# Kernel tuning notes

Measured on AMD Instinct MI355X. Metric: run time of the kernel, lower is better.

Reference implementation:

```python
import jax, jax.numpy as jnp
import numpy as np

N_ATOMS = 100000
N_BONDS = 2000000
F = 32  # fixed feature width implied by hardcoded MLP input dims


def _linear_init(key, din, dout):
    kw, kb = jax.random.split(key)
    s = 1.0 / np.sqrt(din)
    w = jax.random.uniform(kw, (din, dout), jnp.float32, -s, s)
    b = jax.random.uniform(kb, (dout,), jnp.float32, -s, s)
    return w, b


def _mlp(x, w1, b1, w2, b2, w3, b3):
    # Linear(din,64)-SELU-Linear(64,64)-SELU-Linear(64,32)-SELU
    x = jax.nn.selu(x @ w1 + b1)
    x = jax.nn.selu(x @ w2 + b2)
    return jax.nn.selu(x @ w3 + b3)


def setup_inputs() -> dict:
    key = jax.random.key(0)
    ks = jax.random.split(key, 14)
    inp = {
        "bonds": jax.random.normal(ks[0], (N_BONDS, F), jnp.float32),
        "bond_atom_1": jax.random.randint(ks[1], (N_BONDS,), 0, N_ATOMS, jnp.int32),
        "bond_atom_2": jax.random.randint(ks[2], (N_BONDS,), 0, N_ATOMS, jnp.int32),
        "atoms": jax.random.normal(ks[3], (N_ATOMS, F), jnp.float32),
        "state": jax.random.normal(ks[4], (1, F), jnp.float32),
    }
    # phi_e: 128 -> 64 -> 64 -> 32
    inp["e_w1"], inp["e_b1"] = _linear_init(ks[5], 128, 64)
    inp["e_w2"], inp["e_b2"] = _linear_init(ks[6], 64, 64)
    inp["e_w3"], inp["e_b3"] = _linear_init(ks[7], 64, 32)
    # phi_v: 96 -> 64 -> 64 -> 32
    inp["v_w1"], inp["v_b1"] = _linear_init(ks[8], 96, 64)
    inp["v_w2"], inp["v_b2"] = _linear_init(ks[9], 64, 64)
    inp["v_w3"], inp["v_b3"] = _linear_init(ks[10], 64, 32)
    # phi_u: 96 -> 64 -> 64 -> 32
    inp["u_w1"], inp["u_b1"] = _linear_init(ks[11], 96, 64)
    inp["u_w2"], inp["u_b2"] = _linear_init(ks[12], 64, 64)
    inp["u_w3"], inp["u_b3"] = _linear_init(ks[13], 64, 32)
    return inp


def reference(bonds, bond_atom_1, bond_atom_2, atoms, state,
              e_w1, e_b1, e_w2, e_b2, e_w3, e_b3,
              v_w1, v_b1, v_w2, v_b2, v_w3, v_b3,
              u_w1, u_b1, u_w2, u_b2, u_w3, u_b3):
    n_bonds = bonds.shape[0]
    n_atoms = atoms.shape[0]
    state_b = jnp.broadcast_to(state, (n_bonds, state.shape[1]))
    # gather atom features per bond endpoint
    a1 = atoms[bond_atom_1]  # [E, F]
    a2 = atoms[bond_atom_2]  # [E, F]
    bonds_new = _mlp(jnp.concatenate([a1, a2, bonds, state_b], axis=1),
                     e_w1, e_b1, e_w2, e_b2, e_w3, e_b3)  # [E, 32]
    # scatter-add bond messages back to atom 1, normalize by bond count
    b2a = jax.ops.segment_sum(bonds_new, bond_atom_1, num_segments=n_atoms)  # [N, 32]
    cnt = jax.ops.segment_sum(jnp.ones((n_bonds,), bonds_new.dtype), bond_atom_1,
                              num_segments=n_atoms)  # [N]
    b2a = b2a / cnt[:, None]
    state_a = jnp.broadcast_to(state, (n_atoms, state.shape[1]))
    atoms_new = _mlp(jnp.concatenate([b2a, atoms, state_a], axis=1),
                     v_w1, v_b1, v_w2, v_b2, v_w3, v_b3)  # [N, 32]
    state_new = _mlp(jnp.concatenate([jnp.mean(bonds_new, axis=0, keepdims=True),
                                      jnp.mean(atoms_new, axis=0, keepdims=True),
                                      state], axis=1),
                     u_w1, u_b1, u_w2, u_b2, u_w3, u_b3)  # [1, 32]
    return bonds_new, atoms_new, state_new
```

## Files before the change

kernel.cpp:

```cpp
#include <hip/hip_runtime.h>
#include <math.h>

typedef __attribute__((ext_vector_type(4))) int    int4v;
typedef __attribute__((ext_vector_type(4))) float  float4v;
typedef __attribute__((ext_vector_type(8))) __bf16 bf16x8;

#define SCAN_BLK 1024
#define EBLK 512

static constexpr float SELU_SCALE = 1.0507009873554805f;
static constexpr float SELU_ALPHA = 1.6732632423543772f;

__device__ __forceinline__ float selu_f(float x) {
    const float sa = SELU_SCALE * SELU_ALPHA;
    float e = __expf(x);
    return x > 0.0f ? SELU_SCALE * x : fmaf(sa, e, -sa);
}

__device__ __forceinline__ unsigned short f2bf(float f) {
    uint32_t u = __builtin_bit_cast(uint32_t, f);
    return (unsigned short)((u + 0x7FFFu + ((u >> 16) & 1u)) >> 16);
}

__device__ __forceinline__ uint32_t pk2(float a, float b) {
    uint32_t r;
    asm("v_cvt_pk_bf16_f32 %0, %1, %2" : "=v"(r) : "v"(a), "v"(b));
    return r;
}

__device__ __forceinline__ float4v mfma_bf16(int4v a, int4v b, float4v c) {
    return __builtin_amdgcn_mfma_f32_16x16x32_bf16(
        __builtin_bit_cast(bf16x8, a), __builtin_bit_cast(bf16x8, b), c, 0, 0, 0);
}


__global__ __launch_bounds__(256) void cnt_kernel(const int* __restrict__ ba1,
                                                  int* __restrict__ cnt, int nb) {
    for (int e = blockIdx.x * 256 + threadIdx.x; e < nb; e += gridDim.x * 256)
        atomicAdd(cnt + ba1[e], 1);
}

__global__ __launch_bounds__(SCAN_BLK) void scan_block_kernel(const int* __restrict__ cnt,
                                                              int* __restrict__ excl,
                                                              int* __restrict__ bsums, int na) {
    __shared__ int tmp[SCAN_BLK];
    const int t = threadIdx.x;
    const int base = blockIdx.x * SCAN_BLK;
    const int v = (base + t < na) ? cnt[base + t] : 0;
    tmp[t] = v;
    __syncthreads();
    for (int off = 1; off < SCAN_BLK; off <<= 1) {
        const int add = (t >= off) ? tmp[t - off] : 0;
        __syncthreads();
        tmp[t] += add;
        __syncthreads();
    }
    if (base + t < na) excl[base + t] = tmp[t] - v;
    if (t == SCAN_BLK - 1) bsums[blockIdx.x] = tmp[t];
}

__global__ void scan_tops_kernel(const int* __restrict__ bsums, int* __restrict__ bases,
                                 int nblocks) {
    if (threadIdx.x == 0 && blockIdx.x == 0) {
        int s = 0;
        for (int bk = 0; bk < nblocks; ++bk) { bases[bk] = s; s += bsums[bk]; }
    }
}

__global__ __launch_bounds__(256) void wcur_init_kernel(const int* __restrict__ excl,
                                                        const int* __restrict__ bases,
                                                        int* __restrict__ wcur, int na) {
    const int a = blockIdx.x * 256 + threadIdx.x;
    if (a < na) wcur[a] = bases[a >> 10] + excl[a];
}


__global__ void bias_prep_kernel(const float* __restrict__ state,
                                 const float* __restrict__ ew1, const float* __restrict__ eb1,
                                 const float* __restrict__ vw1, const float* __restrict__ vb1,
                                 float* __restrict__ ebias, float* __restrict__ vbias) {
    const int t = threadIdx.x;
    if (t >= 64) return;
    if (blockIdx.x == 0) {
        float acc = eb1[t];
        for (int k = 0; k < 32; ++k) acc = fmaf(state[k], ew1[(96 + k) * 64 + t], acc);
        ebias[t] = acc;
    } else {
        float acc = vb1[t];
        for (int k = 0; k < 32; ++k) acc = fmaf(state[k], vw1[(64 + k) * 64 + t], acc);
        vbias[t] = acc;
    }
}


__global__ __launch_bounds__(256) void aprep_kernel(const float* __restrict__ atoms,
                                                    unsigned short* __restrict__ abf,
                                                    int nel8) {
    const int i = blockIdx.x * 256 + threadIdx.x;
    if (i >= nel8) return;
    const float* p = atoms + (size_t)i * 8;
    uint4 v;
    v.x = pk2(p[0], p[1]); v.y = pk2(p[2], p[3]);
    v.z = pk2(p[4], p[5]); v.w = pk2(p[6], p[7]);
    *(uint4*)(abf + (size_t)i * 8) = v;
}

__global__ __launch_bounds__(256) void wprep_kernel(
    const float* __restrict__ ew1, const float* __restrict__ ew2, const float* __restrict__ ew3,
    const float* __restrict__ vw1, const float* __restrict__ vw2, const float* __restrict__ vw3,
    unsigned short* __restrict__ wfe, unsigned short* __restrict__ wfv)
{
    const int idx = blockIdx.x * 256 + threadIdx.x;
    if (idx >= 44 * 64) return;
    const int fid = idx >> 6, lane = idx & 63;
    const int b = lane & 15, g = lane >> 4;
    const float* W; int N, t, c;
    if (fid < 12)      { W = ew1; N = 64; t = fid / 3;        c = fid % 3; }
    else if (fid < 20) { W = ew2; N = 64; t = (fid - 12) / 2; c = (fid - 12) % 2; }
    else if (fid < 24) { W = ew3; N = 32; t = (fid - 20) / 2; c = (fid - 20) % 2; }
    else if (fid < 32) { W = vw1; N = 64; t = (fid - 24) / 2; c = (fid - 24) % 2; }
    else if (fid < 40) { W = vw2; N = 64; t = (fid - 32) / 2; c = (fid - 32) % 2; }
    else               { W = vw3; N = 32; t = (fid - 40) / 2; c = (fid - 40) % 2; }
    unsigned short* dst = (fid < 24) ? (wfe + fid * 512) : (wfv + (fid - 24) * 512);
    for (int j = 0; j < 8; ++j) {
        const float w = W[(size_t)(32 * c + 8 * g + j) * N + 16 * t + b];
        dst[lane * 8 + j] = f2bf(w);
    }
}


__global__ __launch_bounds__(EBLK, 8) void phi_e_mfma(
    const float* __restrict__ bonds, const int* __restrict__ ba1, const int* __restrict__ ba2,
    const unsigned short* __restrict__ abf,
    const unsigned short* __restrict__ wfe, const float* __restrict__ ebias,
    const float* __restrict__ eb2, const float* __restrict__ eb3,
    float* __restrict__ out, int* __restrict__ wcur, int* __restrict__ list, int nb)
{
    __shared__ __align__(16) char lds[25344 + (EBLK / 64) * 2048];
    {
        const uint4* src = (const uint4*)wfe;
        uint4* dst = (uint4*)lds;
        #pragma unroll
        for (int i = 0; i < 3; ++i) dst[threadIdx.x + i * EBLK] = src[threadIdx.x + i * EBLK];
        float* bd = (float*)(lds + 24576);
        const int t = threadIdx.x;
        if (t < 64)        bd[t] = ebias[t];
        else if (t < 128)  bd[t] = eb2[t - 64];
        else if (t < 160)  bd[t] = eb3[t - 128];
    }
    __syncthreads();

    const char* wl = lds;
    const float* bias_l = (const float*)(lds + 24576);
    const int tid = threadIdx.x;
    const int wid = tid >> 6, lane = tid & 63;
    const int b = lane & 15, g = lane >> 4;
    char* hb = lds + 25344 + wid * 2048;
    const uint32_t swz = (uint32_t)((b & 7) << 4);
    const uint32_t row = (uint32_t)(b * 128);
    const uint32_t loff = (uint32_t)(lane * 16);

    const int ntile = (nb + 15) >> 4;
    const int stride = gridDim.x * (EBLK / 64);

    for (int m = blockIdx.x * (EBLK / 64) + wid; m < ntile; m += stride) {
        const int e0 = m << 4;
        const int er = min(e0 + b, nb - 1);
        const int i1 = ba1[er], i2 = ba2[er];

        if (g == 0 && e0 + b < nb) {
            const int pos = atomicAdd(wcur + i1, 1);
            __builtin_nontemporal_store(er, list + pos);
        }

        const int4v xa1 = *(const int4v*)(abf + (size_t)i1 * 32 + 8 * g);
        const int4v xa2 = *(const int4v*)(abf + (size_t)i2 * 32 + 8 * g);
        int4v xb;
        {
            const float* p = bonds + (size_t)er * 32 + 8 * g;
            const float4v u0 = __builtin_nontemporal_load((const float4v*)p);
            const float4v u1 = __builtin_nontemporal_load((const float4v*)p + 1);
            xb[0] = (int)pk2(u0.x, u0.y); xb[1] = (int)pk2(u0.z, u0.w);
            xb[2] = (int)pk2(u1.x, u1.y); xb[3] = (int)pk2(u1.z, u1.w);
        }

        float4v acc[4];
        #pragma unroll
        for (int t = 0; t < 4; ++t) acc[t] = *(const float4v*)(bias_l + 16 * t + 4 * g);
        #pragma unroll
        for (int t = 0; t < 4; ++t) {
            acc[t] = mfma_bf16(*(const int4v*)(wl + (t * 3 + 0) * 1024 + loff), xa1, acc[t]);
            acc[t] = mfma_bf16(*(const int4v*)(wl + (t * 3 + 1) * 1024 + loff), xa2, acc[t]);
            acc[t] = mfma_bf16(*(const int4v*)(wl + (t * 3 + 2) * 1024 + loff), xb,  acc[t]);
        }
        #pragma unroll
        for (int t = 0; t < 4; ++t) {
            const float s0 = selu_f(acc[t][0]), s1 = selu_f(acc[t][1]);
            const float s2 = selu_f(acc[t][2]), s3 = selu_f(acc[t][3]);
            const uint32_t q = (uint32_t)(t * 32 + g * 8);
            *(uint2*)(hb + row + (q ^ swz)) = make_uint2(pk2(s0, s1), pk2(s2, s3));
        }
        int4v xh0 = *(const int4v*)(hb + row + (((uint32_t)(g * 16)) ^ swz));
        int4v xh1 = *(const int4v*)(hb + row + (((uint32_t)(64 + g * 16)) ^ swz));

        #pragma unroll
        for (int t = 0; t < 4; ++t) acc[t] = *(const float4v*)(bias_l + 64 + 16 * t + 4 * g);
        #pragma unroll
        for (int t = 0; t < 4; ++t) {
            acc[t] = mfma_bf16(*(const int4v*)(wl + (12 + t * 2 + 0) * 1024 + loff), xh0, acc[t]);
            acc[t] = mfma_bf16(*(const int4v*)(wl + (12 + t * 2 + 1) * 1024 + loff), xh1, acc[t]);
        }
        #pragma unroll
        for (int t = 0; t < 4; ++t) {
            const float s0 = selu_f(acc[t][0]), s1 = selu_f(acc[t][1]);
            const float s2 = selu_f(acc[t][2]), s3 = selu_f(acc[t][3]);
            const uint32_t q = (uint32_t)(t * 32 + g * 8);
            *(uint2*)(hb + row + (q ^ swz)) = make_uint2(pk2(s0, s1), pk2(s2, s3));
        }
        xh0 = *(const int4v*)(hb + row + (((uint32_t)(g * 16)) ^ swz));
        xh1 = *(const int4v*)(hb + row + (((uint32_t)(64 + g * 16)) ^ swz));

        float4v acc3[2];
        acc3[0] = *(const float4v*)(bias_l + 128 + 4 * g);
        acc3[1] = *(const float4v*)(bias_l + 128 + 16 + 4 * g);
        #pragma unroll
        for (int t = 0; t < 2; ++t) {
            acc3[t] = mfma_bf16(*(const int4v*)(wl + (20 + t * 2 + 0) * 1024 + loff), xh0, acc3[t]);
            acc3[t] = mfma_bf16(*(const int4v*)(wl + (20 + t * 2 + 1) * 1024 + loff), xh1, acc3[t]);
        }
        if (e0 + b < nb) {
            #pragma unroll
            for (int t = 0; t < 2; ++t) {
                float4v ov;
                ov.x = selu_f(acc3[t][0]); ov.y = selu_f(acc3[t][1]);
                ov.z = selu_f(acc3[t][2]); ov.w = selu_f(acc3[t][3]);
                *(float4v*)(out + (size_t)(e0 + b) * 32 + 16 * t + 4 * g) = ov;
            }
        }
    }
}


__global__ __launch_bounds__(256) void gather_mean_kernel(
    const float* __restrict__ bonds_new, const int* __restrict__ list,
    const int* __restrict__ excl, const int* __restrict__ bases,
    const int* __restrict__ cnt, float* __restrict__ mean,
    float* __restrict__ bpart, int na)
{
    __shared__ float red[4][32];
    const int idx = blockIdx.x * 256 + threadIdx.x;
    const int a = idx >> 3, q = idx & 7;
    float4v s = {0.f, 0.f, 0.f, 0.f};
    int n = 0;
    if (a < na) {
        const int start = bases[a >> 10] + excl[a];
        n = cnt[a];
        const int end = start + n;
        float4v s1 = {0.f, 0.f, 0.f, 0.f};
        float4v s2 = {0.f, 0.f, 0.f, 0.f};
        float4v s3 = {0.f, 0.f, 0.f, 0.f};
        int p = start;
        for (; p + 4 <= end; p += 4) {
            const int e0 = list[p], e1 = list[p + 1], e2 = list[p + 2], e3 = list[p + 3];
            s  += *(const float4v*)(bonds_new + (size_t)e0 * 32 + q * 4);
            s1 += *(const float4v*)(bonds_new + (size_t)e1 * 32 + q * 4);
            s2 += *(const float4v*)(bonds_new + (size_t)e2 * 32 + q * 4);
            s3 += *(const float4v*)(bonds_new + (size_t)e3 * 32 + q * 4);
        }
        for (; p < end; ++p)
            s += *(const float4v*)(bonds_new + (size_t)list[p] * 32 + q * 4);
        s = (s + s1) + (s2 + s3);
    }

    {
        float4v t = s;
        #pragma unroll
        for (int off = 8; off < 64; off <<= 1) {
            t.x += __shfl_xor(t.x, off); t.y += __shfl_xor(t.y, off);
            t.z += __shfl_xor(t.z, off); t.w += __shfl_xor(t.w, off);
        }
        const int wv = threadIdx.x >> 6;
        const int lane = threadIdx.x & 63;
        if (lane < 8) {
            red[wv][lane * 4 + 0] = t.x; red[wv][lane * 4 + 1] = t.y;
            red[wv][lane * 4 + 2] = t.z; red[wv][lane * 4 + 3] = t.w;
        }
        __syncthreads();
        if (threadIdx.x < 32) {
            const int f = threadIdx.x;
            bpart[(size_t)blockIdx.x * 32 + f] =
                red[0][f] + red[1][f] + red[2][f] + red[3][f];
        }
    }

    if (a < na) {
        const float inv = 1.0f / (float)n;
        *(float4v*)(mean + (size_t)a * 32 + q * 4) = s * inv;
    }
}


__global__ __launch_bounds__(1024) void part_reduce_kernel(const float* __restrict__ part,
                                                           float* __restrict__ dst, int nblk) {
    __shared__ float red[32][33];
    const int f = threadIdx.x & 31;
    const int c = threadIdx.x >> 5;
    float s = 0.0f;
    for (int i = c; i < nblk; i += 32) s += part[(size_t)i * 32 + f];
    red[c][f] = s;
    __syncthreads();
    if (threadIdx.x < 32) {
        float t = 0.0f;
        #pragma unroll
        for (int c2 = 0; c2 < 32; ++c2) t += red[c2][threadIdx.x];
        dst[threadIdx.x] = t;
    }
}


__global__ __launch_bounds__(256) void phi_v_mfma(
    const unsigned short* __restrict__ abf, float* __restrict__ out ,
    const unsigned short* __restrict__ wfv, const float* __restrict__ vbias,
    const float* __restrict__ vb2, const float* __restrict__ vb3,
    float* __restrict__ apart, int na)
{
    __shared__ __align__(16) char lds_raw[4 * 2048];
    __shared__ float redv[4][32];
    const int tid = threadIdx.x;
    const int wid = tid >> 6, lane = tid & 63;
    const int b = lane & 15, g = lane >> 4;
    char* hb = lds_raw + wid * 2048;
    const uint32_t swz = (uint32_t)((b & 7) << 4);
    const uint32_t row = (uint32_t)(b * 128);

    int4v wv1[4][2], wv2[4][2], wv3[2][2];
    #pragma unroll
    for (int t = 0; t < 4; ++t)
        #pragma unroll
        for (int c = 0; c < 2; ++c) {
            wv1[t][c] = *(const int4v*)(wfv + (t * 2 + c) * 512 + lane * 8);
            wv2[t][c] = *(const int4v*)(wfv + (8 + t * 2 + c) * 512 + lane * 8);
        }
    #pragma unroll
    for (int t = 0; t < 2; ++t)
        #pragma unroll
        for (int c = 0; c < 2; ++c)
            wv3[t][c] = *(const int4v*)(wfv + (16 + t * 2 + c) * 512 + lane * 8);

    float ssum[8];
    #pragma unroll
    for (int i = 0; i < 8; ++i) ssum[i] = 0.0f;

    const int ntile = (na + 15) >> 4;
    const int m = blockIdx.x * 4 + wid;
    if (m < ntile) {
        const int a0 = m << 4;
        const int ar = (a0 + b < na) ? (a0 + b) : (na - 1);

        int4v xm;
        {
            const float* p = out + (size_t)ar * 32 + 8 * g;
            const float4v u0 = *(const float4v*)p, u1 = *(const float4v*)(p + 4);
            xm[0] = (int)pk2(u0.x, u0.y); xm[1] = (int)pk2(u0.z, u0.w);
            xm[2] = (int)pk2(u1.x, u1.y); xm[3] = (int)pk2(u1.z, u1.w);
        }
        const int4v xa = *(const int4v*)(abf + (size_t)ar * 32 + 8 * g);

        float4v acc[4];
        #pragma unroll
        for (int t = 0; t < 4; ++t) acc[t] = *(const float4v*)(vbias + 16 * t + 4 * g);
        #pragma unroll
        for (int t = 0; t < 4; ++t) {
            acc[t] = mfma_bf16(wv1[t][0], xm, acc[t]);
            acc[t] = mfma_bf16(wv1[t][1], xa, acc[t]);
        }
        #pragma unroll
        for (int t = 0; t < 4; ++t) {
            const float s0 = selu_f(acc[t][0]), s1 = selu_f(acc[t][1]);
            const float s2 = selu_f(acc[t][2]), s3 = selu_f(acc[t][3]);
            const uint32_t q = (uint32_t)(t * 32 + g * 8);
            *(uint2*)(hb + row + (q ^ swz)) = make_uint2(pk2(s0, s1), pk2(s2, s3));
        }
        int4v xh0 = *(const int4v*)(hb + row + (((uint32_t)(g * 16)) ^ swz));
        int4v xh1 = *(const int4v*)(hb + row + (((uint32_t)(64 + g * 16)) ^ swz));

        #pragma unroll
        for (int t = 0; t < 4; ++t) acc[t] = *(const float4v*)(vb2 + 16 * t + 4 * g);
        #pragma unroll
        for (int t = 0; t < 4; ++t) {
            acc[t] = mfma_bf16(wv2[t][0], xh0, acc[t]);
            acc[t] = mfma_bf16(wv2[t][1], xh1, acc[t]);
        }
        #pragma unroll
        for (int t = 0; t < 4; ++t) {
            const float s0 = selu_f(acc[t][0]), s1 = selu_f(acc[t][1]);
            const float s2 = selu_f(acc[t][2]), s3 = selu_f(acc[t][3]);
            const uint32_t q = (uint32_t)(t * 32 + g * 8);
            *(uint2*)(hb + row + (q ^ swz)) = make_uint2(pk2(s0, s1), pk2(s2, s3));
        }
        xh0 = *(const int4v*)(hb + row + (((uint32_t)(g * 16)) ^ swz));
        xh1 = *(const int4v*)(hb + row + (((uint32_t)(64 + g * 16)) ^ swz));

        float4v acc3[2];
        acc3[0] = *(const float4v*)(vb3 + 4 * g);
        acc3[1] = *(const float4v*)(vb3 + 16 + 4 * g);
        #pragma unroll
        for (int t = 0; t < 2; ++t) {
            acc3[t] = mfma_bf16(wv3[t][0], xh0, acc3[t]);
            acc3[t] = mfma_bf16(wv3[t][1], xh1, acc3[t]);
        }
        if (a0 + b < na) {
            #pragma unroll
            for (int t = 0; t < 2; ++t) {
                const float o0 = selu_f(acc3[t][0]), o1 = selu_f(acc3[t][1]);
                const float o2 = selu_f(acc3[t][2]), o3 = selu_f(acc3[t][3]);
                float4v ov; ov.x = o0; ov.y = o1; ov.z = o2; ov.w = o3;
                *(float4v*)(out + (size_t)(a0 + b) * 32 + 16 * t + 4 * g) = ov;
                ssum[t * 4 + 0] += o0; ssum[t * 4 + 1] += o1;
                ssum[t * 4 + 2] += o2; ssum[t * 4 + 3] += o3;
            }
        }
    }

    #pragma unroll
    for (int i = 0; i < 8; ++i) {
        float v = ssum[i];
        v += __shfl_xor(v, 1); v += __shfl_xor(v, 2);
        v += __shfl_xor(v, 4); v += __shfl_xor(v, 8);
        if (b == 0) redv[wid][16 * (i >> 2) + 4 * g + (i & 3)] = v;
    }
    __syncthreads();
    if (tid < 32)
        apart[(size_t)blockIdx.x * 32 + tid] =
            redv[0][tid] + redv[1][tid] + redv[2][tid] + redv[3][tid];
}


__global__ __launch_bounds__(128) void phi_u_kernel(
    const float* __restrict__ bsum, const float* __restrict__ asum,
    const float* __restrict__ state,
    const float* __restrict__ w1, const float* __restrict__ b1,
    const float* __restrict__ w2, const float* __restrict__ b2,
    const float* __restrict__ w3, const float* __restrict__ b3,
    float* __restrict__ out, float inv_nb, float inv_na)
{
    __shared__ float x[96];
    __shared__ float hs[64];
    const int t = threadIdx.x;
    if (t < 32)       x[t] = bsum[t] * inv_nb;
    else if (t < 64)  x[t] = asum[t - 32] * inv_na;
    else if (t < 96)  x[t] = state[t - 64];
    __syncthreads();
    if (t < 64) {
        float acc = b1[t];
        for (int k = 0; k < 96; ++k) acc = fmaf(x[k], w1[k * 64 + t], acc);
        hs[t] = selu_f(acc);
    }
    __syncthreads();
    float acc2 = 0.0f;
    if (t < 64) {
        acc2 = b2[t];
        for (int k = 0; k < 64; ++k) acc2 = fmaf(hs[k], w2[k * 64 + t], acc2);
        acc2 = selu_f(acc2);
    }
    __syncthreads();
    if (t < 64) hs[t] = acc2;
    __syncthreads();
    if (t < 32) {
        float acc = b3[t];
        for (int k = 0; k < 64; ++k) acc = fmaf(hs[k], w3[k * 32 + t], acc);
        out[t] = selu_f(acc);
    }
}

extern "C" void kernel_launch(void* const* d_in, const int* in_sizes, int n_in,
                              void* d_out, int out_size, void* d_ws, size_t ws_size,
                              hipStream_t stream) {
    const float* bonds = (const float*)d_in[0];
    const int*   ba1   = (const int*)d_in[1];
    const int*   ba2   = (const int*)d_in[2];
    const float* atoms = (const float*)d_in[3];
    const float* state = (const float*)d_in[4];
    const float* ew1 = (const float*)d_in[5];  const float* eb1 = (const float*)d_in[6];
    const float* ew2 = (const float*)d_in[7];  const float* eb2 = (const float*)d_in[8];
    const float* ew3 = (const float*)d_in[9];  const float* eb3 = (const float*)d_in[10];
    const float* vw1 = (const float*)d_in[11]; const float* vb1 = (const float*)d_in[12];
    const float* vw2 = (const float*)d_in[13]; const float* vb2 = (const float*)d_in[14];
    const float* vw3 = (const float*)d_in[15]; const float* vb3 = (const float*)d_in[16];
    const float* uw1 = (const float*)d_in[17]; const float* ub1 = (const float*)d_in[18];
    const float* uw2 = (const float*)d_in[19]; const float* ub2 = (const float*)d_in[20];
    const float* uw3 = (const float*)d_in[21]; const float* ub3 = (const float*)d_in[22];

    const int nb = in_sizes[1];
    const int na = in_sizes[3] / 32;
    const int nscan = (na + SCAN_BLK - 1) / SCAN_BLK;
    const int ngather = ((na * 8) + 255) / 256;
    const int ntv = (na + 15) / 16;
    const int nvblk = (ntv + 3) / 4;

    float* out       = (float*)d_out;
    float* bonds_out = out;
    float* atoms_out = out + (size_t)nb * 32;
    float* state_out = atoms_out + (size_t)na * 32;

    char* ws = (char*)d_ws;
    size_t off = 0;
    auto alloc = [&](size_t bytes) { char* p = ws + off; off += (bytes + 255) & ~(size_t)255; return p; };
    int*   cnt   = (int*)alloc((size_t)na * 4);
    const size_t zero_bytes = off;
    float* bsum  = (float*)alloc(32 * 4);
    float* asum  = (float*)alloc(32 * 4);
    float* ebias = (float*)alloc(64 * 4);
    float* vbias = (float*)alloc(64 * 4);
    int*   excl  = (int*)alloc((size_t)na * 4);
    int*   bsums = (int*)alloc(128 * 4);
    int*   bases = (int*)alloc(128 * 4);
    int*   wcur  = (int*)alloc((size_t)na * 4);
    int*   list  = (int*)alloc((size_t)nb * 4);
    float* bpart = (float*)alloc((size_t)ngather * 32 * 4);
    float* apart = (float*)alloc((size_t)nvblk * 32 * 4);
    unsigned short* wfe = (unsigned short*)alloc(24 * 512 * 2);
    unsigned short* wfv = (unsigned short*)alloc(20 * 512 * 2);
    unsigned short* abf = (unsigned short*)alloc((size_t)na * 32 * 2);

    (void)hipMemsetAsync(d_ws, 0, zero_bytes, stream);

    bias_prep_kernel<<<2, 64, 0, stream>>>(state, ew1, eb1, vw1, vb1, ebias, vbias);
    wprep_kernel<<<(44 * 64 + 255) / 256, 256, 0, stream>>>(ew1, ew2, ew3, vw1, vw2, vw3,
                                                            wfe, wfv);
    aprep_kernel<<<(na * 4 + 255) / 256, 256, 0, stream>>>(atoms, abf, na * 4);

    cnt_kernel<<<2048, 256, 0, stream>>>(ba1, cnt, nb);
    scan_block_kernel<<<nscan, SCAN_BLK, 0, stream>>>(cnt, excl, bsums, na);
    scan_tops_kernel<<<1, 64, 0, stream>>>(bsums, bases, nscan);
    wcur_init_kernel<<<(na + 255) / 256, 256, 0, stream>>>(excl, bases, wcur, na);

    phi_e_mfma<<<1024, EBLK, 0, stream>>>(bonds, ba1, ba2, abf, wfe, ebias, eb2, eb3,
                                          bonds_out, wcur, list, nb);

    gather_mean_kernel<<<ngather, 256, 0, stream>>>(bonds_out, list, excl, bases, cnt,
                                                    atoms_out, bpart, na);
    part_reduce_kernel<<<1, 1024, 0, stream>>>(bpart, bsum, ngather);

    phi_v_mfma<<<nvblk, 256, 0, stream>>>(abf, atoms_out, wfv, vbias, vb2, vb3,
                                          apart, na);
    part_reduce_kernel<<<1, 1024, 0, stream>>>(apart, asum, nvblk);

    phi_u_kernel<<<1, 128, 0, stream>>>(bsum, asum, state,
                                        uw1, ub1, uw2, ub2, uw3, ub3,
                                        state_out, 1.0f / (float)nb, 1.0f / (float)na);
}
```

Before: 442.6 us.

## Scatter bf16 bond outputs into atom-sorted buffer for contiguous segment gather

In the edge MLP kernel, each bond's output is also written as bf16 into a permuted buffer at its CSR slot, instead of writing an index list. The segment-mean kernel then reads contiguous bf16 rows rather than doing indirect fp32 gathers through the list. The last-layer weights are kept in registers, which shrinks the LDS footprint. The trade-off is an extra scattered write per bond and bf16 rounding in the segment sums, and the path depends on having enough workspace.

```diff
diff --git a/kernel.cpp b/kernel.cpp
--- a/kernel.cpp
+++ b/kernel.cpp
@@ -1,6 +1,7 @@
 #include <hip/hip_runtime.h>
 #include <math.h>
 
+typedef __attribute__((ext_vector_type(2))) unsigned int uint2v;
 typedef __attribute__((ext_vector_type(4))) int    int4v;
 typedef __attribute__((ext_vector_type(4))) float  float4v;
 typedef __attribute__((ext_vector_type(8))) __bf16 bf16x8;
@@ -26,6 +27,13 @@
     uint32_t r;
     asm("v_cvt_pk_bf16_f32 %0, %1, %2" : "=v"(r) : "v"(a), "v"(b));
     return r;
+}
+
+__device__ __forceinline__ float bflo(uint32_t u) {
+    return __builtin_bit_cast(float, u << 16);
+}
+__device__ __forceinline__ float bfhi(uint32_t u) {
+    return __builtin_bit_cast(float, u & 0xFFFF0000u);
 }
 
 __device__ __forceinline__ float4v mfma_bf16(int4v a, int4v b, float4v c) {
@@ -129,20 +137,21 @@
 }
 
 
+template<bool PERM>
 __global__ __launch_bounds__(EBLK, 8) void phi_e_mfma(
     const float* __restrict__ bonds, const int* __restrict__ ba1, const int* __restrict__ ba2,
     const unsigned short* __restrict__ abf,
     const unsigned short* __restrict__ wfe, const float* __restrict__ ebias,
     const float* __restrict__ eb2, const float* __restrict__ eb3,
-    float* __restrict__ out, int* __restrict__ wcur, int* __restrict__ list, int nb)
+    float* __restrict__ out, unsigned short* __restrict__ perm,
+    int* __restrict__ wcur, int* __restrict__ list, int nb)
 {
-    __shared__ __align__(16) char lds[25344 + (EBLK / 64) * 2048];
+    __shared__ __align__(16) char lds[21248 + (EBLK / 64) * 2048];
     {
         const uint4* src = (const uint4*)wfe;
         uint4* dst = (uint4*)lds;
-        #pragma unroll
-        for (int i = 0; i < 3; ++i) dst[threadIdx.x + i * EBLK] = src[threadIdx.x + i * EBLK];
-        float* bd = (float*)(lds + 24576);
+        for (int i = threadIdx.x; i < 1280; i += EBLK) dst[i] = src[i];
+        float* bd = (float*)(lds + 20480);
         const int t = threadIdx.x;
         if (t < 64)        bd[t] = ebias[t];
         else if (t < 128)  bd[t] = eb2[t - 64];
@@ -151,14 +160,21 @@
     __syncthreads();
 
     const char* wl = lds;
-    const float* bias_l = (const float*)(lds + 24576);
+    const float* bias_l = (const float*)(lds + 20480);
     const int tid = threadIdx.x;
     const int wid = tid >> 6, lane = tid & 63;
     const int b = lane & 15, g = lane >> 4;
-    char* hb = lds + 25344 + wid * 2048;
+    char* hb = lds + 21248 + wid * 2048;
     const uint32_t swz = (uint32_t)((b & 7) << 4);
     const uint32_t row = (uint32_t)(b * 128);
     const uint32_t loff = (uint32_t)(lane * 16);
+
+    int4v we3[2][2];
+    #pragma unroll
+    for (int t = 0; t < 2; ++t)
+        #pragma unroll
+        for (int c = 0; c < 2; ++c)
+            we3[t][c] = *(const int4v*)(wfe + (20 + t * 2 + c) * 512 + lane * 8);
 
     const int ntile = (nb + 15) >> 4;
     const int stride = gridDim.x * (EBLK / 64);
@@ -168,9 +184,10 @@
         const int er = min(e0 + b, nb - 1);
         const int i1 = ba1[er], i2 = ba2[er];
 
-        if (g == 0 && e0 + b < nb) {
-            const int pos = atomicAdd(wcur + i1, 1);
-            __builtin_nontemporal_store(er, list + pos);
+        int pos = 0;
+        if (lane < 16 && e0 + b < nb) {
+            pos = atomicAdd(wcur + i1, 1);
+            if (!PERM) __builtin_nontemporal_store(er, list + pos);
         }
 
         const int4v xa1 = *(const int4v*)(abf + (size_t)i1 * 32 + 8 * g);
@@ -225,18 +242,86 @@
         acc3[1] = *(const float4v*)(bias_l + 128 + 16 + 4 * g);
         #pragma unroll
         for (int t = 0; t < 2; ++t) {
-            acc3[t] = mfma_bf16(*(const int4v*)(wl + (20 + t * 2 + 0) * 1024 + loff), xh0, acc3[t]);
-            acc3[t] = mfma_bf16(*(const int4v*)(wl + (20 + t * 2 + 1) * 1024 + loff), xh1, acc3[t]);
-        }
+            acc3[t] = mfma_bf16(we3[t][0], xh0, acc3[t]);
+            acc3[t] = mfma_bf16(we3[t][1], xh1, acc3[t]);
+        }
+
+        if (PERM) pos = __shfl(pos, b);
+
         if (e0 + b < nb) {
             #pragma unroll
             for (int t = 0; t < 2; ++t) {
-                float4v ov;
-                ov.x = selu_f(acc3[t][0]); ov.y = selu_f(acc3[t][1]);
-                ov.z = selu_f(acc3[t][2]); ov.w = selu_f(acc3[t][3]);
-                *(float4v*)(out + (size_t)(e0 + b) * 32 + 16 * t + 4 * g) = ov;
+                const float o0 = selu_f(acc3[t][0]), o1 = selu_f(acc3[t][1]);
+                const float o2 = selu_f(acc3[t][2]), o3 = selu_f(acc3[t][3]);
+                float4v ov; ov.x = o0; ov.y = o1; ov.z = o2; ov.w = o3;
+                if (PERM) {
+                    __builtin_nontemporal_store(ov,
+                        (float4v*)(out + (size_t)(e0 + b) * 32 + 16 * t + 4 * g));
+                    uint2v pv; pv.x = pk2(o0, o1); pv.y = pk2(o2, o3);
+                    *((uint2v*)(perm + (size_t)pos * 32) + (4 * t + g)) = pv;
+                } else {
+                    *(float4v*)(out + (size_t)(e0 + b) * 32 + 16 * t + 4 * g) = ov;
+                }
             }
         }
+    }
+}
+
+
+__global__ __launch_bounds__(256) void gather_perm_kernel(
+    const unsigned short* __restrict__ perm,
+    const int* __restrict__ excl, const int* __restrict__ bases,
+    const int* __restrict__ cnt, float* __restrict__ mean,
+    float* __restrict__ bpart, int na)
+{
+    __shared__ float red[4][32];
+    const int idx = blockIdx.x * 256 + threadIdx.x;
+    const int a = idx >> 3, q = idx & 7;
+    float4v s = {0.f, 0.f, 0.f, 0.f};
+    int n = 0;
+    if (a < na) {
+        const int start = bases[a >> 10] + excl[a];
+        n = cnt[a];
+        float4v s1 = {0.f, 0.f, 0.f, 0.f};
+        const unsigned short* base = perm + (size_t)start * 32 + q * 4;
+        int j = 0;
+        for (; j + 2 <= n; j += 2) {
+            const uint2v v0 = *(const uint2v*)(base + (size_t)j * 32);
+            const uint2v v1 = *(const uint2v*)(base + (size_t)(j + 1) * 32);
+            s.x += bflo(v0.x);  s.y += bfhi(v0.x);  s.z += bflo(v0.y);  s.w += bfhi(v0.y);
+            s1.x += bflo(v1.x); s1.y += bfhi(v1.x); s1.z += bflo(v1.y); s1.w += bfhi(v1.y);
+        }
+        if (j < n) {
+            const uint2v v0 = *(const uint2v*)(base + (size_t)j * 32);
+            s.x += bflo(v0.x); s.y += bfhi(v0.x); s.z += bflo(v0.y); s.w += bfhi(v0.y);
+        }
+        s += s1;
+    }
+
+    {
+        float4v t = s;
+        #pragma unroll
+        for (int off = 8; off < 64; off <<= 1) {
+            t.x += __shfl_xor(t.x, off); t.y += __shfl_xor(t.y, off);
+            t.z += __shfl_xor(t.z, off); t.w += __shfl_xor(t.w, off);
+        }
+        const int wv = threadIdx.x >> 6;
+        const int lane = threadIdx.x & 63;
+        if (lane < 8) {
+            red[wv][lane * 4 + 0] = t.x; red[wv][lane * 4 + 1] = t.y;
+            red[wv][lane * 4 + 2] = t.z; red[wv][lane * 4 + 3] = t.w;
+        }
+        __syncthreads();
+        if (threadIdx.x < 32) {
+            const int f = threadIdx.x;
+            bpart[(size_t)blockIdx.x * 32 + f] =
+                red[0][f] + red[1][f] + red[2][f] + red[3][f];
+        }
+    }
+
+    if (a < na) {
+        const float inv = 1.0f / (float)n;
+        *(float4v*)(mean + (size_t)a * 32 + q * 4) = s * inv;
     }
 }
 
@@ -257,21 +342,16 @@
         n = cnt[a];
         const int end = start + n;
         float4v s1 = {0.f, 0.f, 0.f, 0.f};
-        float4v s2 = {0.f, 0.f, 0.f, 0.f};
-        float4v s3 = {0.f, 0.f, 0.f, 0.f};
         int p = start;
-        for (; p + 4 <= end; p += 4) {
-            const int e0 = list[p], e1 = list[p + 1], e2 = list[p + 2], e3 = list[p + 3];
+        for (; p + 2 <= end; p += 2) {
+            const int e0 = list[p], e1 = list[p + 1];
             s  += *(const float4v*)(bonds_new + (size_t)e0 * 32 + q * 4);
             s1 += *(const float4v*)(bonds_new + (size_t)e1 * 32 + q * 4);
-            s2 += *(const float4v*)(bonds_new + (size_t)e2 * 32 + q * 4);
-            s3 += *(const float4v*)(bonds_new + (size_t)e3 * 32 + q * 4);
         }
         for (; p < end; ++p)
             s += *(const float4v*)(bonds_new + (size_t)list[p] * 32 + q * 4);
-        s = (s + s1) + (s2 + s3);
-    }
-
+        s += s1;
+    }
     {
         float4v t = s;
         #pragma unroll
@@ -292,7 +372,6 @@
                 red[0][f] + red[1][f] + red[2][f] + red[3][f];
         }
     }
-
     if (a < na) {
         const float inv = 1.0f / (float)n;
         *(float4v*)(mean + (size_t)a * 32 + q * 4) = s * inv;
@@ -522,6 +601,9 @@
     unsigned short* wfe = (unsigned short*)alloc(24 * 512 * 2);
     unsigned short* wfv = (unsigned short*)alloc(20 * 512 * 2);
     unsigned short* abf = (unsigned short*)alloc((size_t)na * 32 * 2);
+    const size_t perm_bytes = (size_t)nb * 32 * 2;
+    const bool use_perm = (off + perm_bytes) <= ws_size;
+    unsigned short* perm = use_perm ? (unsigned short*)alloc(perm_bytes) : (unsigned short*)list;
 
     (void)hipMemsetAsync(d_ws, 0, zero_bytes, stream);
 
@@ -535,11 +617,17 @@
     scan_tops_kernel<<<1, 64, 0, stream>>>(bsums, bases, nscan);
     wcur_init_kernel<<<(na + 255) / 256, 256, 0, stream>>>(excl, bases, wcur, na);
 
-    phi_e_mfma<<<1024, EBLK, 0, stream>>>(bonds, ba1, ba2, abf, wfe, ebias, eb2, eb3,
-                                          bonds_out, wcur, list, nb);
-
-    gather_mean_kernel<<<ngather, 256, 0, stream>>>(bonds_out, list, excl, bases, cnt,
-                                                    atoms_out, bpart, na);
+    if (use_perm) {
+        phi_e_mfma<true><<<1024, EBLK, 0, stream>>>(bonds, ba1, ba2, abf, wfe, ebias, eb2, eb3,
+                                                    bonds_out, perm, wcur, list, nb);
+        gather_perm_kernel<<<ngather, 256, 0, stream>>>(perm, excl, bases, cnt,
+                                                        atoms_out, bpart, na);
+    } else {
+        phi_e_mfma<false><<<1024, EBLK, 0, stream>>>(bonds, ba1, ba2, abf, wfe, ebias, eb2, eb3,
+                                                     bonds_out, perm, wcur, list, nb);
+        gather_mean_kernel<<<ngather, 256, 0, stream>>>(bonds_out, list, excl, bases, cnt,
+                                                        atoms_out, bpart, na);
+    }
     part_reduce_kernel<<<1, 1024, 0, stream>>>(bpart, bsum, ngather);
 
     phi_v_mfma<<<nvblk, 256, 0, stream>>>(abf, atoms_out, wfv, vbias, vb2, vb3,
```

New measurement: 480.6 us. +8.6%, slower.
